# Performance work log

Measured on AMD Instinct MI355X. Metric: run time of the kernel, lower is better.

Reference implementation:

```python
import jax, jax.numpy as jnp
import numpy as np

NUM_HEADS = 32
NUM_KV_GROUPS = 8


def _rope(x, cos, sin):
    # x: [B, H, S, hd]; cos/sin: [S_max, hd]
    S, hd = x.shape[2], x.shape[3]
    x1, x2 = x[..., : hd // 2], x[..., hd // 2 :]
    rotated = jnp.concatenate((-x2, x1), axis=-1)
    c = cos[:S][None, None]
    s = sin[:S][None, None]
    return (x * c + rotated * s).astype(x.dtype)


def setup_inputs() -> dict:
    key = jax.random.key(0)
    ks = jax.random.split(key, 8)
    B, S, D = 2, 2048, 2048
    H, G = NUM_HEADS, NUM_KV_GROUPS
    hd = D // H
    scale = 1.0 / np.sqrt(D)
    return {
        "inputs": jax.random.normal(ks[0], (B, S, D), jnp.float32),
        "mask": jnp.zeros((S, S), jnp.bool_),  # note: original masked_fill is not in-place -> mask unused
        "cos": jax.random.uniform(ks[1], (S, hd), jnp.float32),
        "sin": jax.random.uniform(ks[2], (S, hd), jnp.float32),
        "Wq": jax.random.normal(ks[3], (D, H * hd), jnp.float32) * scale,
        "Wk": jax.random.normal(ks[4], (D, G * hd), jnp.float32) * scale,
        "Wv": jax.random.normal(ks[5], (D, G * hd), jnp.float32) * scale,
        "Wo": jax.random.normal(ks[6], (H * hd, H * hd), jnp.float32) * scale,
    }


def reference(inputs, mask, cos, sin, Wq, Wk, Wv, Wo):
    B, S, D = inputs.shape
    H, G = NUM_HEADS, NUM_KV_GROUPS
    hd = Wq.shape[1] // H
    group_size = H // G

    q = (inputs @ Wq).reshape(B, S, H, hd).transpose(0, 2, 1, 3)  # [B,H,S,hd]
    k = (inputs @ Wk).reshape(B, S, G, hd).transpose(0, 2, 1, 3)  # [B,G,S,hd]
    v = (inputs @ Wv).reshape(B, S, G, hd).transpose(0, 2, 1, 3)

    q = _rope(q, cos, sin)
    k = _rope(k, cos, sin)

    k = jnp.repeat(k, group_size, axis=1)  # [B,H,S,hd]
    v = jnp.repeat(v, group_size, axis=1)

    scores = jnp.einsum("bhqd,bhkd->bhqk", q, k)
    # NOTE: original uses non-inplace masked_fill whose result is discarded,
    # so faithfully NO mask is applied.
    attn = jax.nn.softmax(scores / jnp.sqrt(jnp.float32(hd)).astype(scores.dtype), axis=-1)
    ctx = jnp.einsum("bhqk,bhkd->bhqd", attn, v)
    ctx = ctx.transpose(0, 2, 1, 3).reshape(B, S, H * hd)
    return ctx @ Wo
```

## Files before the change

kernel.cpp:

```cpp
#include <hip/hip_runtime.h>
#include <stdint.h>

typedef __attribute__((ext_vector_type(8))) short short8;
typedef __attribute__((ext_vector_type(4))) short short4v;
typedef __attribute__((ext_vector_type(4))) float float4v;
typedef __attribute__((ext_vector_type(2))) unsigned uint2v;

__device__ __forceinline__ float bf2f(short s) {
  union { unsigned u; float f; } x;
  x.u = ((unsigned)(unsigned short)s) << 16;
  return x.f;
}
__device__ __forceinline__ short f2bf(float f) {
  union { float f; unsigned u; } x;
  x.f = f;
  unsigned r = x.u + 0x7fffu + ((x.u >> 16) & 1u);
  return (short)(r >> 16);
}
__device__ __forceinline__ float fexp2(float x) {
#if __has_builtin(__builtin_amdgcn_exp2f)
  return __builtin_amdgcn_exp2f(x);
#else
  float r;
  asm("v_exp_f32 %0, %1" : "=v"(r) : "v"(x));
  return r;
#endif
}
__device__ __forceinline__ void glds16(const void* g, void* l) {
  __builtin_amdgcn_global_load_lds(
      (const __attribute__((address_space(1))) void*)g,
      (__attribute__((address_space(3))) void*)l, 16, 0, 0);
}
__device__ __forceinline__ void bar() { __builtin_amdgcn_s_barrier(); }

__device__ __forceinline__ void transpose_tile(
    const float* __restrict__ src, short* __restrict__ dst, int R, int C,
    int r0, int c0) {
  __shared__ short t[64 * 72];
  const int tid = threadIdx.x;
#pragma unroll
  for (int r = 0; r < 2; ++r) {
    int c = r * 256 + tid;
    int row = c >> 3, col8 = (c & 7) * 8;
    const float4v a = *(const float4v*)&src[(long)(r0 + row) * C + c0 + col8];
    const float4v b = *(const float4v*)&src[(long)(r0 + row) * C + c0 + col8 + 4];
    short8 v;
#pragma unroll
    for (int e = 0; e < 4; ++e) { v[e] = f2bf(a[e]); v[e + 4] = f2bf(b[e]); }
    *(short8*)&t[row * 72 + col8] = v;
  }
  __syncthreads();
#pragma unroll
  for (int r = 0; r < 2; ++r) {
    int c = r * 256 + tid;
    int orow = c >> 3, ocol8 = (c & 7) * 8;
    short8 w;
#pragma unroll
    for (int e = 0; e < 8; ++e) w[e] = t[(ocol8 + e) * 72 + orow];
    *(short8*)&dst[(long)(c0 + orow) * R + r0 + ocol8] = w;
  }
}

__global__ __launch_bounds__(256) void prep(
    const float* __restrict__ X, short* __restrict__ Xb,
    const float* __restrict__ Wq, const float* __restrict__ Wk,
    const float* __restrict__ Wv, short* __restrict__ WT) {
  const int id = blockIdx.x;
  if (id < 4096) {
    const long i = ((long)id * 256 + threadIdx.x) * 8;
    const float4v a = *(const float4v*)&X[i];
    const float4v b = *(const float4v*)&X[i + 4];
    short8 v;
#pragma unroll
    for (int e = 0; e < 4; ++e) { v[e] = f2bf(a[e]); v[e + 4] = f2bf(b[e]); }
    *(short8*)&Xb[i] = v;
  } else {
    const int r = id - 4096;
    const int z = r >> 10, bx = r & 31, by = (r >> 5) & 31;
    const float* src = z == 0 ? Wq : (z == 1 ? Wk : Wv);
    const int C = z == 0 ? 2048 : 512;
    if (bx * 64 < C) {
      short* dst = WT + (z == 0 ? 0 : (z == 1 ? 2048 * 2048 : 2560 * 2048));
      transpose_tile(src, dst, 2048, C, by * 64, bx * 64);
    }
  }
}

__global__ __launch_bounds__(256) void transpose_f2b(
    const float* __restrict__ src, short* __restrict__ dst, int R, int C) {
  transpose_tile(src, dst, R, C, blockIdx.y * 64, blockIdx.x * 64);
}

__global__ __launch_bounds__(256) void vtrans(const short* __restrict__ Y,
                                              short* __restrict__ Vt,
                                              int ld, int col0) {
  const int bg = blockIdx.y;
  const int b = bg >> 3, gk = bg & 7;
  const int s0 = blockIdx.x * 64;
  __shared__ short t[64 * 72];
  const int tid = threadIdx.x;
#pragma unroll
  for (int r = 0; r < 2; ++r) {
    int c = r * 256 + tid;
    int row = c >> 3, col8 = (c & 7) * 8;
    short8 v = *(const short8*)&Y[(long)(b * 2048 + s0 + row) * ld + col0 + gk * 64 + col8];
    *(short8*)&t[row * 72 + col8] = v;
  }
  __syncthreads();
#pragma unroll
  for (int r = 0; r < 2; ++r) {
    int c = r * 256 + tid;
    int d = c >> 3, s8 = (c & 7) * 8;
    short8 w;
#pragma unroll
    for (int e = 0; e < 8; ++e) w[e] = t[(s8 + e) * 72 + d];
    *(short8*)&Vt[((long)bg * 64 + d) * 2048 + s0 + s8] = w;
  }
}

template <int MODE>
__global__ __launch_bounds__(256) void gemm_bt(
    const short* __restrict__ A, const short* __restrict__ BT,
    float* __restrict__ Cf, short* __restrict__ Qr, short* __restrict__ Kr,
    short* __restrict__ YV, const float* __restrict__ cosp,
    const float* __restrict__ sinp, int M, int N, int K) {
  (void)M;
  __shared__ short As[128 * 32];
  __shared__ short Bs[128 * 32];
  const int tid = threadIdx.x;
  const int wave = tid >> 6, lane = tid & 63;
  const int g = lane >> 4, lr = lane & 15;
  const int wr = wave >> 1, wc = wave & 1;
  const int m0 = blockIdx.y << 7, n0 = blockIdx.x << 7;

  float4v acc[4][4];
#pragma unroll
  for (int i = 0; i < 4; ++i)
#pragma unroll
    for (int j = 0; j < 4; ++j) acc[i][j] = (float4v)0.f;

  for (int kt = 0; kt < K; kt += 32) {
#pragma unroll
    for (int r = 0; r < 2; ++r) {
      const int cb = r * 256 + wave * 64;
      const int c = cb + lane;
      const int row = c >> 2, kc = c & 3;
      glds16(A + (long)(m0 + row) * K + kt + kc * 8, As + cb * 8);
      glds16(BT + (long)(n0 + row) * K + kt + kc * 8, Bs + cb * 8);
    }
    __syncthreads();
    short8 af[4], bfr[4];
#pragma unroll
    for (int i = 0; i < 4; ++i)
      af[i] = *(const short8*)&As[(wr * 64 + i * 16 + lr) * 32 + g * 8];
#pragma unroll
    for (int j = 0; j < 4; ++j)
      bfr[j] = *(const short8*)&Bs[(wc * 64 + j * 16 + lr) * 32 + g * 8];
#pragma unroll
    for (int i = 0; i < 4; ++i)
#pragma unroll
      for (int j = 0; j < 4; ++j)
        acc[i][j] = __builtin_amdgcn_mfma_f32_16x16x32_bf16(af[i], bfr[j], acc[i][j], 0, 0, 0);
    __syncthreads();
  }

  if constexpr (MODE == 1) {
    const int h = (n0 + wc * 64) >> 6;
#pragma unroll
    for (int i = 0; i < 4; ++i)
#pragma unroll
      for (int t = 0; t < 4; ++t) {
        const int r = m0 + wr * 64 + i * 16 + g * 4 + t;
        const int s = r & 2047, bb = r >> 11;
        if (h < 40) {
          const float sc = h < 32 ? 0.18033688011112043f : 1.0f;
          short* base = h < 32
              ? Qr + ((long)(bb * 32 + h) * 2048 + s) * 64
              : Kr + ((long)(bb * 8 + (h - 32)) * 2048 + s) * 64;
          const float* cr = cosp + s * 64;
          const float* sr = sinp + s * 64;
#pragma unroll
          for (int j = 0; j < 2; ++j) {
            const int d = j * 16 + lr;
            const float x1 = acc[i][j][t];
            const float x2 = acc[i][j + 2][t];
            base[d] = f2bf((x1 * cr[d] - x2 * sr[d]) * sc);
            base[d + 32] = f2bf((x2 * cr[d + 32] + x1 * sr[d + 32]) * sc);
          }
        } else {
          short* base = YV + ((long)bb * 2048 + s) * 512 + (h - 40) * 64;
#pragma unroll
          for (int j = 0; j < 4; ++j) base[j * 16 + lr] = f2bf(acc[i][j][t]);
        }
      }
  } else {
#pragma unroll
    for (int i = 0; i < 4; ++i)
#pragma unroll
      for (int j = 0; j < 4; ++j)
#pragma unroll
        for (int t = 0; t < 4; ++t) {
          const int r = m0 + wr * 64 + i * 16 + g * 4 + t;
          const int cc = n0 + wc * 64 + j * 16 + lr;
          Cf[(long)r * N + cc] = acc[i][j][t];
        }
  }
}

__global__ __launch_bounds__(512, 4) void attn_kernel(
    const short* __restrict__ Qr, const short* __restrict__ Kr,
    const short* __restrict__ Vt, short* __restrict__ Ctx) {
  constexpr int S = 2048;
  constexpr int NIT = 32;
  const int bh = blockIdx.y;
  const int b = bh >> 5, h = bh & 31;
  const int gk = h >> 2;
  const int q0 = blockIdx.x << 8;
  const int tid = threadIdx.x;
  const int w = tid >> 6, lane = tid & 63;
  const int g = lane >> 4, lr = lane & 15;
  const int b8 = lr & 7;
  const int qrow = w * 16 + lr;

  __shared__ short Ks[2][64 * 64];
  __shared__ short Vs[2][64 * 64];
  __shared__ short Ps[128 * 64];

  const short* Qb = Qr + (long)(b * 32 + h) * S * 64;
  const short* Kb = Kr + (long)(b * 8 + gk) * S * 64;
  const short* Vb = Vt + (long)(b * 8 + gk) * 64 * S;

  const int ko0 = lr * 64 + ((0 + g) ^ b8) * 8;
  const int ko1 = lr * 64 + ((4 + g) ^ b8) * 8;
  int vo[2], pr[2], pw[4];
#pragma unroll
  for (int ks = 0; ks < 2; ++ks) {
    vo[ks] = lr * 64 + ((ks * 4 + g) ^ b8) * 8;
    pr[ks] = qrow * 64 + ((ks * 4 + g) ^ b8) * 8;
  }
#pragma unroll
  for (int i = 0; i < 4; ++i)
    pw[i] = qrow * 64 + ((2 * i + (g >> 1)) ^ b8) * 8 + (g & 1) * 4;

  const int srow = tid >> 3, sl = tid & 7;
  const long koff = (long)srow * 64 + (sl ^ (srow & 7)) * 8;
  const long voff = (long)srow * S + (sl ^ (srow & 7)) * 8;

  short8 qf[2][2];
#pragma unroll
  for (int qh = 0; qh < 2; ++qh) {
    qf[qh][0] = *(const short8*)&Qb[(long)(q0 + qh * 128 + qrow) * 64 + g * 8];
    qf[qh][1] = *(const short8*)&Qb[(long)(q0 + qh * 128 + qrow) * 64 + 32 + g * 8];
  }

  const short8 ones = (short8)(short)0x3F80;
  float4v lacc[2];
  float4v oacc[2][4];
#pragma unroll
  for (int qh = 0; qh < 2; ++qh) {
    lacc[qh] = (float4v)0.f;
#pragma unroll
    for (int di = 0; di < 4; ++di) oacc[qh][di] = (float4v)0.f;
  }

  glds16(Kb + koff, &Ks[0][w * 512]);
  glds16(Vb + voff, &Vs[0][w * 512]);

  for (int it = 0; it < NIT; ++it) {
    const int buf = it & 1;
    if (it + 1 < NIT) {
      glds16(Kb + (long)(it + 1) * 64 * 64 + koff, &Ks[buf ^ 1][w * 512]);
      glds16(Vb + (it + 1) * 64 + voff, &Vs[buf ^ 1][w * 512]);
      asm volatile("s_waitcnt vmcnt(2)" ::: "memory");
    } else {
      asm volatile("s_waitcnt vmcnt(0)" ::: "memory");
    }
    __builtin_amdgcn_sched_barrier(0);
    bar();

    short8 kf[8];
#pragma unroll
    for (int i = 0; i < 4; ++i) {
      kf[i] = *(const short8*)&Ks[buf][ko0 + i * 1024];
      kf[4 + i] = *(const short8*)&Ks[buf][ko1 + i * 1024];
    }

#pragma unroll
    for (int qh = 0; qh < 2; ++qh) {
      float4v sacc[4];
#pragma unroll
      for (int i = 0; i < 4; ++i) sacc[i] = (float4v)0.f;
      __builtin_amdgcn_s_setprio(1);
#pragma unroll
      for (int i = 0; i < 4; ++i)
        sacc[i] = __builtin_amdgcn_mfma_f32_16x16x32_bf16(kf[i], qf[qh][0], sacc[i], 0, 0, 0);
#pragma unroll
      for (int i = 0; i < 4; ++i)
        sacc[i] = __builtin_amdgcn_mfma_f32_16x16x32_bf16(kf[4 + i], qf[qh][1], sacc[i], 0, 0, 0);
      __builtin_amdgcn_s_setprio(0);

#pragma unroll
      for (int i = 0; i < 4; ++i) {
        union { float f; unsigned u; } a0, a1, a2, a3;
        a0.f = fexp2(sacc[i][0]);
        a1.f = fexp2(sacc[i][1]);
        a2.f = fexp2(sacc[i][2]);
        a3.f = fexp2(sacc[i][3]);
        const unsigned d0 = __builtin_amdgcn_perm(a1.u + 0x8000u, a0.u + 0x8000u, 0x07060302u);
        const unsigned d1 = __builtin_amdgcn_perm(a3.u + 0x8000u, a2.u + 0x8000u, 0x07060302u);
        *(uint2v*)&Ps[pw[i]] = (uint2v){d0, d1};
      }

      __builtin_amdgcn_s_setprio(1);
#pragma unroll
      for (int ks = 0; ks < 2; ++ks) {
        const short8 pf = *(const short8*)&Ps[pr[ks]];
        lacc[qh] = __builtin_amdgcn_mfma_f32_16x16x32_bf16(ones, pf, lacc[qh], 0, 0, 0);
#pragma unroll
        for (int di = 0; di < 4; ++di) {
          const short8 vf = *(const short8*)&Vs[buf][vo[ks] + di * 1024];
          oacc[qh][di] = __builtin_amdgcn_mfma_f32_16x16x32_bf16(vf, pf, oacc[qh][di], 0, 0, 0);
        }
      }
      __builtin_amdgcn_s_setprio(0);
    }
    bar();
  }

#pragma unroll
  for (int qh = 0; qh < 2; ++qh) {
    const float inv = 1.f / lacc[qh][0];
    const int q = q0 + qh * 128 + qrow;
#pragma unroll
    for (int di = 0; di < 4; ++di) {
      short4v o;
#pragma unroll
      for (int t = 0; t < 4; ++t) o[t] = f2bf(oacc[qh][di][t] * inv);
      *(short4v*)&Ctx[(long)(b * S + q) * 2048 + h * 64 + di * 16 + g * 4] = o;
    }
  }
}

extern "C" void kernel_launch(void* const* d_in, const int* in_sizes, int n_in,
                              void* d_out, int out_size, void* d_ws, size_t ws_size,
                              hipStream_t stream) {
  (void)in_sizes; (void)n_in; (void)out_size; (void)ws_size;
  const float* X    = (const float*)d_in[0];
  const float* cosp = (const float*)d_in[2];
  const float* sinp = (const float*)d_in[3];
  const float* Wq   = (const float*)d_in[4];
  const float* Wk   = (const float*)d_in[5];
  const float* Wv   = (const float*)d_in[6];
  const float* Wo   = (const float*)d_in[7];
  float* out = (float*)d_out;
  char* ws = (char*)d_ws;

  short* Xb = (short*)(ws + 0);
  short* WT = (short*)(ws + 16777216);
  short* Y  = (short*)(ws + 29360128);
  short* Qr = (short*)(ws + 46137344);
  short* Kr = (short*)(ws + 62914560);
  short* YV = (short*)(ws + 67108864);
  short* Vt = (short*)(ws + 71303168);

  prep<<<7168, 256, 0, stream>>>(X, Xb, Wq, Wk, Wv, WT);

  gemm_bt<1><<<dim3(24, 32), 256, 0, stream>>>(
      Xb, WT, nullptr, Qr, Kr, YV, cosp, sinp, 4096, 3072, 2048);

  transpose_f2b<<<dim3(32, 32), 256, 0, stream>>>(Wo, WT, 2048, 2048);

  vtrans<<<dim3(32, 16), 256, 0, stream>>>(YV, Vt, 512, 0);

  attn_kernel<<<dim3(8, 64), 512, 0, stream>>>(Qr, Kr, Vt, Y);

  gemm_bt<2><<<dim3(16, 32), 256, 0, stream>>>(
      Y, WT, out, nullptr, nullptr, nullptr, nullptr, nullptr, 4096, 2048, 2048);
}
```

Measured before the change: 355.4 us.

## Rewrite GEMM with 256x256 tiles, double-buffered swizzled LDS, and hoist V loads

Replaces the 128x128 single-buffered GEMM with a 512-thread kernel that computes 256x256 tiles and uses K-step 64. LDS is double-buffered, and async global-to-LDS loads overlap MFMA work. An XOR swizzle on LDS columns avoids bank conflicts. In the attention kernel, V fragments are loaded from LDS once per iteration, before the Q-half loop, instead of once per half. The larger tiles raise reuse and cut barrier count, but they use much more LDS and registers and launch fewer blocks (192 and 128), which may underfill the 256 CUs.

```diff
diff --git a/kernel.cpp b/kernel.cpp
--- a/kernel.cpp
+++ b/kernel.cpp
@@ -119,58 +119,90 @@
 }
 
 template <int MODE>
-__global__ __launch_bounds__(256) void gemm_bt(
+__global__ __launch_bounds__(512, 1) void gemm2(
     const short* __restrict__ A, const short* __restrict__ BT,
     float* __restrict__ Cf, short* __restrict__ Qr, short* __restrict__ Kr,
     short* __restrict__ YV, const float* __restrict__ cosp,
     const float* __restrict__ sinp, int M, int N, int K) {
   (void)M;
-  __shared__ short As[128 * 32];
-  __shared__ short Bs[128 * 32];
+  __shared__ short As[2][16384];
+  __shared__ short Bs[2][16384];
   const int tid = threadIdx.x;
-  const int wave = tid >> 6, lane = tid & 63;
+  const int w = tid >> 6, lane = tid & 63;
   const int g = lane >> 4, lr = lane & 15;
-  const int wr = wave >> 1, wc = wave & 1;
-  const int m0 = blockIdx.y << 7, n0 = blockIdx.x << 7;
-
-  float4v acc[4][4];
-#pragma unroll
-  for (int i = 0; i < 4; ++i)
+  const int wm = w >> 2, wn = w & 3;
+  const int m0 = blockIdx.y << 8, n0 = blockIdx.x << 8;
+
+  const int r0 = tid >> 3;
+  const int scol = ((tid & 7) << 3) ^ (((r0 >> 2) & 1) << 4) ^ (((r0 >> 3) & 1) << 5);
+  const long aoff = (long)(m0 + r0) * K + scol;
+  const long boff = (long)(n0 + r0) * K + scol;
+
+  const int swz = (((lr >> 2) & 1) << 4) | (((lr >> 3) & 1) << 5);
+  const int acol0 = (g << 3) ^ swz;
+  const int acol1 = (32 + (g << 3)) ^ swz;
+  const int abase = (wm * 128 + lr) * 64;
+  const int bbase = (wn * 64 + lr) * 64;
+
+  float4v acc[8][4];
+#pragma unroll
+  for (int i = 0; i < 8; ++i)
 #pragma unroll
     for (int j = 0; j < 4; ++j) acc[i][j] = (float4v)0.f;
 
-  for (int kt = 0; kt < K; kt += 32) {
-#pragma unroll
-    for (int r = 0; r < 2; ++r) {
-      const int cb = r * 256 + wave * 64;
-      const int c = cb + lane;
-      const int row = c >> 2, kc = c & 3;
-      glds16(A + (long)(m0 + row) * K + kt + kc * 8, As + cb * 8);
-      glds16(BT + (long)(n0 + row) * K + kt + kc * 8, Bs + cb * 8);
-    }
-    __syncthreads();
-    short8 af[4], bfr[4];
-#pragma unroll
-    for (int i = 0; i < 4; ++i)
-      af[i] = *(const short8*)&As[(wr * 64 + i * 16 + lr) * 32 + g * 8];
-#pragma unroll
-    for (int j = 0; j < 4; ++j)
-      bfr[j] = *(const short8*)&Bs[(wc * 64 + j * 16 + lr) * 32 + g * 8];
-#pragma unroll
-    for (int i = 0; i < 4; ++i)
-#pragma unroll
-      for (int j = 0; j < 4; ++j)
-        acc[i][j] = __builtin_amdgcn_mfma_f32_16x16x32_bf16(af[i], bfr[j], acc[i][j], 0, 0, 0);
-    __syncthreads();
+#define STAGE_A(l, buf, kg)                                          \
+  glds16(A + aoff + (long)(l) * 64 * K + (kg),                       \
+         &As[(buf)][(l) * 4096 + w * 512])
+#define STAGE_B(l, buf, kg)                                          \
+  glds16(BT + boff + (long)(l) * 64 * K + (kg),                      \
+         &Bs[(buf)][(l) * 4096 + w * 512])
+
+  const int NT = K >> 6;
+#pragma unroll
+  for (int l = 0; l < 4; ++l) { STAGE_A(l, 0, 0); STAGE_B(l, 0, 0); }
+  asm volatile("s_waitcnt vmcnt(0)" ::: "memory");
+  __builtin_amdgcn_sched_barrier(0);
+  bar();
+
+  for (int t = 0; t < NT; ++t) {
+    const int buf = t & 1;
+    if (t + 1 < NT) {
+      const long kg = (long)(t + 1) << 6;
+#pragma unroll
+      for (int l = 0; l < 4; ++l) { STAGE_A(l, buf ^ 1, kg); STAGE_B(l, buf ^ 1, kg); }
+    }
+    const short* const Asb = As[buf];
+    const short* const Bsb = Bs[buf];
+    short8 bR[4][2];
+#pragma unroll
+    for (int j = 0; j < 4; ++j) {
+      bR[j][0] = *(const short8*)&Bsb[bbase + j * 1024 + acol0];
+      bR[j][1] = *(const short8*)&Bsb[bbase + j * 1024 + acol1];
+    }
+    __builtin_amdgcn_s_setprio(1);
+#pragma unroll
+    for (int i = 0; i < 8; ++i) {
+      const short8 a0 = *(const short8*)&Asb[abase + i * 1024 + acol0];
+      const short8 a1 = *(const short8*)&Asb[abase + i * 1024 + acol1];
+#pragma unroll
+      for (int j = 0; j < 4; ++j) {
+        acc[i][j] = __builtin_amdgcn_mfma_f32_16x16x32_bf16(a0, bR[j][0], acc[i][j], 0, 0, 0);
+        acc[i][j] = __builtin_amdgcn_mfma_f32_16x16x32_bf16(a1, bR[j][1], acc[i][j], 0, 0, 0);
+      }
+    }
+    __builtin_amdgcn_s_setprio(0);
+    asm volatile("s_waitcnt vmcnt(0)" ::: "memory");
+    __builtin_amdgcn_sched_barrier(0);
+    bar();
   }
 
   if constexpr (MODE == 1) {
-    const int h = (n0 + wc * 64) >> 6;
-#pragma unroll
-    for (int i = 0; i < 4; ++i)
+    const int h = (n0 + wn * 64) >> 6;
+#pragma unroll
+    for (int i = 0; i < 8; ++i)
 #pragma unroll
       for (int t = 0; t < 4; ++t) {
-        const int r = m0 + wr * 64 + i * 16 + g * 4 + t;
+        const int r = m0 + wm * 128 + i * 16 + g * 4 + t;
         const int s = r & 2047, bb = r >> 11;
         if (h < 40) {
           const float sc = h < 32 ? 0.18033688011112043f : 1.0f;
@@ -195,16 +227,18 @@
       }
   } else {
 #pragma unroll
-    for (int i = 0; i < 4; ++i)
+    for (int i = 0; i < 8; ++i)
 #pragma unroll
       for (int j = 0; j < 4; ++j)
 #pragma unroll
         for (int t = 0; t < 4; ++t) {
-          const int r = m0 + wr * 64 + i * 16 + g * 4 + t;
-          const int cc = n0 + wc * 64 + j * 16 + lr;
+          const int r = m0 + wm * 128 + i * 16 + g * 4 + t;
+          const int cc = n0 + wn * 64 + j * 16 + lr;
           Cf[(long)r * N + cc] = acc[i][j][t];
         }
   }
+#undef STAGE_A
+#undef STAGE_B
 }
 
 __global__ __launch_bounds__(512, 4) void attn_kernel(
@@ -278,12 +312,17 @@
     __builtin_amdgcn_sched_barrier(0);
     bar();
 
-    short8 kf[8];
+    short8 kf[8], vf[8];
 #pragma unroll
     for (int i = 0; i < 4; ++i) {
       kf[i] = *(const short8*)&Ks[buf][ko0 + i * 1024];
       kf[4 + i] = *(const short8*)&Ks[buf][ko1 + i * 1024];
     }
+#pragma unroll
+    for (int ks = 0; ks < 2; ++ks)
+#pragma unroll
+      for (int di = 0; di < 4; ++di)
+        vf[ks * 4 + di] = *(const short8*)&Vs[buf][vo[ks] + di * 1024];
 
 #pragma unroll
     for (int qh = 0; qh < 2; ++qh) {
@@ -317,10 +356,8 @@
         const short8 pf = *(const short8*)&Ps[pr[ks]];
         lacc[qh] = __builtin_amdgcn_mfma_f32_16x16x32_bf16(ones, pf, lacc[qh], 0, 0, 0);
 #pragma unroll
-        for (int di = 0; di < 4; ++di) {
-          const short8 vf = *(const short8*)&Vs[buf][vo[ks] + di * 1024];
-          oacc[qh][di] = __builtin_amdgcn_mfma_f32_16x16x32_bf16(vf, pf, oacc[qh][di], 0, 0, 0);
-        }
+        for (int di = 0; di < 4; ++di)
+          oacc[qh][di] = __builtin_amdgcn_mfma_f32_16x16x32_bf16(vf[ks * 4 + di], pf, oacc[qh][di], 0, 0, 0);
       }
       __builtin_amdgcn_s_setprio(0);
     }
@@ -365,7 +402,7 @@
 
   prep<<<7168, 256, 0, stream>>>(X, Xb, Wq, Wk, Wv, WT);
 
-  gemm_bt<1><<<dim3(24, 32), 256, 0, stream>>>(
+  gemm2<1><<<dim3(12, 16), 512, 0, stream>>>(
       Xb, WT, nullptr, Qr, Kr, YV, cosp, sinp, 4096, 3072, 2048);
 
   transpose_f2b<<<dim3(32, 32), 256, 0, stream>>>(Wo, WT, 2048, 2048);
@@ -374,6 +411,6 @@
 
   attn_kernel<<<dim3(8, 64), 512, 0, stream>>>(Qr, Kr, Vt, Y);
 
-  gemm_bt<2><<<dim3(16, 32), 256, 0, stream>>>(
+  gemm2<2><<<dim3(8, 16), 512, 0, stream>>>(
       Y, WT, out, nullptr, nullptr, nullptr, nullptr, nullptr, 4096, 2048, 2048);
 }
```

Result: slower. 498.0 us (+40.1%).
